# Performance work log

Measured on AMD Instinct MI355X. Metric: run time of the kernel, lower is better.

The kernel has to match this reference:

```python
import jax, jax.numpy as jnp
import numpy as np

IN_DIM, HIDDEN_DIM, LATENT_DIM = 512, 1024, 256
B, N = 64, 1024


def setup_inputs() -> dict:
    key = jax.random.key(0)
    ks = jax.random.split(key, 8)
    x = jax.random.normal(ks[0], (B, N, IN_DIM), dtype=jnp.float32)
    a = jax.random.uniform(ks[1], (B, N, N), dtype=jnp.float32)
    s1 = 1.0 / np.sqrt(IN_DIM)
    s2 = 1.0 / np.sqrt(HIDDEN_DIM)
    W1 = jax.random.uniform(ks[2], (HIDDEN_DIM, IN_DIM), jnp.float32, -s1, s1)
    b1 = jax.random.uniform(ks[3], (HIDDEN_DIM,), jnp.float32, -s1, s1)
    W_mu = jax.random.uniform(ks[4], (LATENT_DIM, HIDDEN_DIM), jnp.float32, -s2, s2)
    b_mu = jax.random.uniform(ks[5], (LATENT_DIM,), jnp.float32, -s2, s2)
    W_lv = jax.random.uniform(ks[6], (LATENT_DIM, HIDDEN_DIM), jnp.float32, -s2, s2)
    b_lv = jax.random.uniform(ks[7], (LATENT_DIM,), jnp.float32, -s2, s2)
    return {"x": x, "a": a, "W1": W1, "b1": b1, "W_mu": W_mu, "b_mu": b_mu,
            "W_lv": W_lv, "b_lv": b_lv}


def normalize_adj(a):
    # A_hat = A + I; D^{-1/2} A_hat D^{-1/2} expressed as row/col scaling
    n = a.shape[-1]
    a_hat = a + jnp.eye(n, dtype=a.dtype)
    deg = a_hat.sum(axis=-1)                      # [B, N]
    d = (deg + 1e-8) ** -0.5                      # [B, N]
    return a_hat * d[..., :, None] * d[..., None, :]


def reference(x, a, W1, b1, W_mu, b_mu, W_lv, b_lv):
    a_norm = normalize_adj(a)                     # [B, N, N]
    h = jnp.einsum('bnm,bmd->bnd', a_norm, x)     # message passing
    h = jax.nn.relu(jnp.einsum('bnd,hd->bnh', h, W1) + b1)
    mu = jnp.einsum('bnh,lh->bnl', h, W_mu) + b_mu
    logvar = jnp.einsum('bnh,lh->bnl', h, W_lv) + b_lv
    return (mu, logvar)
```

## Files before the change

kernel.cpp:

```cpp
#include <hip/hip_runtime.h>
#include <hip/hip_bf16.h>
#include <type_traits>

typedef unsigned short u16;
typedef __attribute__((ext_vector_type(8))) short s16x8;
typedef __attribute__((ext_vector_type(4))) float f32x4;

__device__ __forceinline__ u16 f2bf(float f) {
    union { float f; unsigned u; } c; c.f = f;
    unsigned r = c.u + 0x7fffu + ((c.u >> 16) & 1u);
    return (u16)(r >> 16);
}

__device__ __forceinline__ void gld_lds16(const u16* g, u16* l) {
    __builtin_amdgcn_global_load_lds(
        (const __attribute__((address_space(1))) void*)g,
        (__attribute__((address_space(3))) void*)l, 16, 0, 0);
}

template<bool CVT>
__global__ __launch_bounds__(256) void rowsum_kernel(const float* __restrict__ a,
                                                     float* __restrict__ dsc,
                                                     u16* __restrict__ ab) {
    const int wave = threadIdx.x >> 6, lane = threadIdx.x & 63;
    const long row = (long)blockIdx.x * 4 + wave;
    const int diag = (int)(row & 1023);
    const float4* a4 = (const float4*)(a + row * 1024);
    float s = 0.f;
    #pragma unroll
    for (int i = 0; i < 4; ++i) {
        float4 v = a4[i * 64 + lane];
        s += v.x + v.y + v.z + v.w;
        if (CVT) {
            const int c0 = (i * 64 + lane) * 4;
            float e[4] = {v.x, v.y, v.z, v.w};
            if (diag >= c0 && diag < c0 + 4) e[diag - c0] += 1.0f;
            union { u16 u[4]; uint2 w; } cv;
            cv.u[0] = f2bf(e[0]); cv.u[1] = f2bf(e[1]);
            cv.u[2] = f2bf(e[2]); cv.u[3] = f2bf(e[3]);
            *(uint2*)(ab + row * 1024 + c0) = cv.w;
        }
    }
    #pragma unroll
    for (int off = 32; off > 0; off >>= 1) s += __shfl_down(s, off, 64);
    if (lane == 0) dsc[row] = rsqrtf(s + 1.0f + 1e-8f);
}

__global__ __launch_bounds__(256) void xst_kernel(const float* __restrict__ x,
                                                  const float* __restrict__ dsc,
                                                  u16* __restrict__ xst) {
    __shared__ u16 ls[64][65];
    const int b  = blockIdx.z;
    const int n0 = blockIdx.x * 64;
    const int j0 = blockIdx.y * 64;
    const int t  = threadIdx.x;
    {
        int jj = t >> 4, nn = (t & 15) * 4;
        #pragma unroll
        for (int it = 0; it < 4; ++it, jj += 16) {
            float dj = dsc[b * 1024 + j0 + jj];
            float4 v = *(const float4*)(x + ((long)(b * 1024 + j0 + jj)) * 512 + n0 + nn);
            ls[jj][nn + 0] = f2bf(v.x * dj);
            ls[jj][nn + 1] = f2bf(v.y * dj);
            ls[jj][nn + 2] = f2bf(v.z * dj);
            ls[jj][nn + 3] = f2bf(v.w * dj);
        }
    }
    __syncthreads();
    {
        int nn = t >> 2;
        int jv = (t & 3) * 8;
        #pragma unroll
        for (int it = 0; it < 2; ++it, jv += 32) {
            union { u16 u[8]; uint4 w; } cv;
            #pragma unroll
            for (int u = 0; u < 8; ++u) cv.u[u] = ls[jv + u][nn];
            *(uint4*)(xst + ((long)b * 512 + n0 + nn) * 1024 + j0 + jv) = cv.w;
        }
    }
}

__global__ __launch_bounds__(256) void cvt_weights(const float* __restrict__ W1,
                                                   const float* __restrict__ Wmu,
                                                   const float* __restrict__ Wlv,
                                                   u16* __restrict__ w1b,
                                                   u16* __restrict__ wml) {
    int i = blockIdx.x * 256 + threadIdx.x;
    w1b[i] = f2bf(W1[i]);
    wml[i] = f2bf(i < 262144 ? Wmu[i] : Wlv[i - 262144]);
}

template<int EPI>
__global__ __launch_bounds__(256) void gemm_lds(
    const u16* __restrict__ A, const u16* __restrict__ Bt,
    int K, long aBStride, long bBStride,
    const float* __restrict__ dsc,
    u16* __restrict__ outb,
    const float* __restrict__ bias0, const float* __restrict__ bias1,
    float* __restrict__ outMu, float* __restrict__ outLv)
{
    __shared__ __align__(16) u16 As[128 * 32];
    __shared__ __align__(16) u16 Bs[128 * 32];
    const int bz = blockIdx.z;
    const u16* Ab = A + (long)bz * aBStride;
    const u16* Bb = Bt + (long)bz * bBStride;
    const int n0 = blockIdx.x * 128, m0 = blockIdx.y * 128;
    const int t = threadIdx.x;
    const int wave = t >> 6, lane = t & 63, quad = lane >> 4, tr = lane & 15;
    const int wm = (wave >> 1) * 64, wn = (wave & 1) * 64;

    const int srowA = wave * 32 + (lane >> 2);
    const int scol  = (lane & 3) * 8;
    u16* ldsA0 = As + wave * 1024;
    u16* ldsB0 = Bs + wave * 1024;

    f32x4 acc[4][4];
    #pragma unroll
    for (int i = 0; i < 4; ++i)
        #pragma unroll
        for (int j = 0; j < 4; ++j) acc[i][j] = (f32x4){0.f, 0.f, 0.f, 0.f};

    for (int k0 = 0; k0 < K; k0 += 32) {
        #pragma unroll
        for (int it = 0; it < 2; ++it) {
            gld_lds16(Ab + (long)(m0 + srowA + it * 16) * K + k0 + scol, ldsA0 + it * 512);
            gld_lds16(Bb + (long)(n0 + srowA + it * 16) * K + k0 + scol, ldsB0 + it * 512);
        }
        __syncthreads();
        s16x8 af[4], bfv[4];
        #pragma unroll
        for (int mi = 0; mi < 4; ++mi)
            af[mi] = *(const s16x8*)&As[(wm + mi * 16 + tr) * 32 + quad * 8];
        #pragma unroll
        for (int ni = 0; ni < 4; ++ni)
            bfv[ni] = *(const s16x8*)&Bs[(wn + ni * 16 + tr) * 32 + quad * 8];
        #pragma unroll
        for (int mi = 0; mi < 4; ++mi)
            #pragma unroll
            for (int ni = 0; ni < 4; ++ni)
                acc[mi][ni] = __builtin_amdgcn_mfma_f32_16x16x32_bf16(af[mi], bfv[ni], acc[mi][ni], 0, 0, 0);
        __syncthreads();
    }

    #pragma unroll
    for (int mi = 0; mi < 4; ++mi) {
        #pragma unroll
        for (int ni = 0; ni < 4; ++ni) {
            const int gn = n0 + wn + ni * 16 + tr;
            #pragma unroll
            for (int r = 0; r < 4; ++r) {
                const int gm = m0 + wm + mi * 16 + quad * 4 + r;
                float v = acc[mi][ni][r];
                if constexpr (EPI == 1) {
                    long row = (long)bz * 1024 + gm;
                    outb[row * 512 + gn] = f2bf(dsc[row] * v);
                } else if constexpr (EPI == 2) {
                    float hv = v + bias0[gn];
                    outb[(long)gm * 1024 + gn] = f2bf(hv > 0.f ? hv : 0.f);
                } else {
                    if (gn < 256) outMu[(long)gm * 256 + gn] = v + bias0[gn];
                    else          outLv[(long)gm * 256 + (gn - 256)] = v + bias1[gn - 256];
                }
            }
        }
    }
}

__global__ __launch_bounds__(256) void gemm_f32a(
    const float* __restrict__ A, const u16* __restrict__ Bt,
    const float* __restrict__ dsc, const float* __restrict__ xin,
    u16* __restrict__ outb)
{
    __shared__ __align__(16) u16 As[128 * 40];
    __shared__ __align__(16) u16 Bs[128 * 40];
    const int bz = blockIdx.z;
    const float* Ab = A + (long)bz * 1024 * 1024;
    const u16* Bb = Bt + (long)bz * 512 * 1024;
    const int n0 = blockIdx.x * 128, m0 = blockIdx.y * 128;
    const int t = threadIdx.x;
    const int wave = t >> 6, lane = t & 63, quad = lane >> 4, tr = lane & 15;
    const int wm = (wave >> 1) * 64, wn = (wave & 1) * 64;
    const int K = 1024;

    f32x4 acc[4][4];
    #pragma unroll
    for (int i = 0; i < 4; ++i)
        #pragma unroll
        for (int j = 0; j < 4; ++j) acc[i][j] = (f32x4){0.f, 0.f, 0.f, 0.f};

    const int mm = t >> 2, kk = (t & 3) * 8;
    for (int k0 = 0; k0 < K; k0 += 32) {
        #pragma unroll
        for (int it = 0; it < 2; ++it) {
            const int r = mm + it * 64;
            const float4* p = (const float4*)(Ab + (long)(m0 + r) * K + k0 + kk);
            float4 v0 = p[0], v1 = p[1];
            union { u16 u[8]; uint4 w; } cv;
            cv.u[0]=f2bf(v0.x); cv.u[1]=f2bf(v0.y); cv.u[2]=f2bf(v0.z); cv.u[3]=f2bf(v0.w);
            cv.u[4]=f2bf(v1.x); cv.u[5]=f2bf(v1.y); cv.u[6]=f2bf(v1.z); cv.u[7]=f2bf(v1.w);
            *(uint4*)&As[r * 40 + kk] = cv.w;
            uint4 v = *(const uint4*)(Bb + (long)(n0 + r) * K + k0 + kk);
            *(uint4*)&Bs[r * 40 + kk] = v;
        }
        __syncthreads();
        s16x8 af[4], bfv[4];
        #pragma unroll
        for (int mi = 0; mi < 4; ++mi)
            af[mi] = *(const s16x8*)&As[(wm + mi * 16 + tr) * 40 + quad * 8];
        #pragma unroll
        for (int ni = 0; ni < 4; ++ni)
            bfv[ni] = *(const s16x8*)&Bs[(wn + ni * 16 + tr) * 40 + quad * 8];
        #pragma unroll
        for (int mi = 0; mi < 4; ++mi)
            #pragma unroll
            for (int ni = 0; ni < 4; ++ni)
                acc[mi][ni] = __builtin_amdgcn_mfma_f32_16x16x32_bf16(af[mi], bfv[ni], acc[mi][ni], 0, 0, 0);
        __syncthreads();
    }
    #pragma unroll
    for (int mi = 0; mi < 4; ++mi)
        #pragma unroll
        for (int ni = 0; ni < 4; ++ni) {
            const int gn = n0 + wn + ni * 16 + tr;
            #pragma unroll
            for (int r = 0; r < 4; ++r) {
                const int gm = m0 + wm + mi * 16 + quad * 4 + r;
                long row = (long)bz * 1024 + gm;
                float di = dsc[row];
                outb[row * 512 + gn] = f2bf(di * (acc[mi][ni][r] + di * xin[row * 512 + gn]));
            }
        }
}

extern "C" void kernel_launch(void* const* d_in, const int* in_sizes, int n_in,
                              void* d_out, int out_size, void* d_ws, size_t ws_size,
                              hipStream_t stream) {
    const float* x   = (const float*)d_in[0];
    const float* a   = (const float*)d_in[1];
    const float* W1  = (const float*)d_in[2];
    const float* b1  = (const float*)d_in[3];
    const float* Wmu = (const float*)d_in[4];
    const float* bmu = (const float*)d_in[5];
    const float* Wlv = (const float*)d_in[6];
    const float* blv = (const float*)d_in[7];
    float* out = (float*)d_out;

    char* base = (char*)d_ws;
    size_t off = 0;
    auto take = [&](size_t bytes) { char* p = base + off; off += (bytes + 255) & ~(size_t)255; return p; };
    float* dsc = (float*)take((size_t)65536 * 4);
    u16*  xst  = (u16*)take((size_t)64 * 512 * 1024 * 2);
    u16*  h    = (u16*)take((size_t)65536 * 512 * 2);
    u16*  hid  = (u16*)take((size_t)65536 * 1024 * 2);
    u16*  w1b  = (u16*)take((size_t)1024 * 512 * 2);
    u16*  wml  = (u16*)take((size_t)512 * 1024 * 2);
    u16*  ab   = (u16*)take((size_t)64 * 1024 * 1024 * 2);
    const bool useAb = (off <= ws_size);

    if (useAb) rowsum_kernel<true ><<<16384, 256, 0, stream>>>(a, dsc, ab);
    else       rowsum_kernel<false><<<16384, 256, 0, stream>>>(a, dsc, nullptr);
    xst_kernel<<<dim3(8, 16, 64), 256, 0, stream>>>(x, dsc, xst);
    cvt_weights<<<2048, 256, 0, stream>>>(W1, Wmu, Wlv, w1b, wml);

    if (useAb)
        gemm_lds<1><<<dim3(4, 8, 64), 256, 0, stream>>>(
            ab, xst, 1024, 1024L * 1024, 512L * 1024,
            dsc, h, nullptr, nullptr, nullptr, nullptr);
    else
        gemm_f32a<<<dim3(4, 8, 64), 256, 0, stream>>>(a, xst, dsc, x, h);

    gemm_lds<2><<<dim3(8, 512, 1), 256, 0, stream>>>(
        h, w1b, 512, 0, 0, nullptr, hid, b1, nullptr, nullptr, nullptr);

    gemm_lds<3><<<dim3(4, 512, 1), 256, 0, stream>>>(
        hid, wml, 1024, 0, 0, nullptr, nullptr, bmu, blv,
        out, out + (size_t)65536 * 256);
}
```

Before: 876.7 us.

## Replace 128x128 GEMM with double-buffered 256x256 tile kernel with swizzled LDS

Replaces the single-buffered 128x128 bf16 MFMA GEMM with a 256x256-tile, 512-thread kernel. It double-buffers LDS through direct global-to-LDS loads, so the next K tile is prefetched while MFMAs run, and uses explicit waitcnt, barriers and setprio to order the work. It also XOR-swizzles the LDS columns to avoid bank conflicts and remaps workgroup IDs for cache locality. The epilogues are simplified with hoisted bias and scale loads. Larger tiles raise data reuse but use more registers (128 accumulator floats per lane), add sync points, and launch fewer workgroups.

```diff
diff --git a/kernel.cpp b/kernel.cpp
--- a/kernel.cpp
+++ b/kernel.cpp
@@ -1,6 +1,5 @@
 #include <hip/hip_runtime.h>
 #include <hip/hip_bf16.h>
-#include <type_traits>
 
 typedef unsigned short u16;
 typedef __attribute__((ext_vector_type(8))) short s16x8;
@@ -91,7 +90,7 @@
 }
 
 template<int EPI>
-__global__ __launch_bounds__(256) void gemm_lds(
+__global__ __launch_bounds__(512, 2) void gemm256(
     const u16* __restrict__ A, const u16* __restrict__ Bt,
     int K, long aBStride, long bBStride,
     const float* __restrict__ dsc,
@@ -99,68 +98,155 @@
     const float* __restrict__ bias0, const float* __restrict__ bias1,
     float* __restrict__ outMu, float* __restrict__ outLv)
 {
-    __shared__ __align__(16) u16 As[128 * 32];
-    __shared__ __align__(16) u16 Bs[128 * 32];
-    const int bz = blockIdx.z;
+    __shared__ __align__(16) u16 As[2][256 * 32];
+    __shared__ __align__(16) u16 Bs[2][256 * 32];
+
+    const int gx = gridDim.x, gy = gridDim.y;
+    const int nwg = gx * gy * gridDim.z;
+    const int fid = (blockIdx.z * gy + blockIdx.y) * gx + blockIdx.x;
+    int swz = fid;
+    if (!(nwg & 7)) swz = (fid & 7) * (nwg >> 3) + (fid >> 3);
+    const int bx  = swz % gx;
+    const int tmp = swz / gx;
+    const int by  = tmp % gy;
+    const int bz  = tmp / gy;
+
     const u16* Ab = A + (long)bz * aBStride;
     const u16* Bb = Bt + (long)bz * bBStride;
-    const int n0 = blockIdx.x * 128, m0 = blockIdx.y * 128;
-    const int t = threadIdx.x;
-    const int wave = t >> 6, lane = t & 63, quad = lane >> 4, tr = lane & 15;
-    const int wm = (wave >> 1) * 64, wn = (wave & 1) * 64;
-
-    const int srowA = wave * 32 + (lane >> 2);
-    const int scol  = (lane & 3) * 8;
-    u16* ldsA0 = As + wave * 1024;
-    u16* ldsB0 = Bs + wave * 1024;
-
-    f32x4 acc[4][4];
-    #pragma unroll
-    for (int i = 0; i < 4; ++i)
+    const int n0 = bx * 256, m0 = by * 256;
+    const int T = (int)threadIdx.x;
+    const int wid = T >> 6, lane = T & 63, quad = lane >> 4, tr = lane & 15;
+    const int wm = (wid >> 2) * 128;
+    const int wn = (wid & 3) * 64;
+    const int NT = K >> 5;
+
+    const int sr   = T >> 2;
+    const int scol = ((T & 3) ^ (sr & 3)) << 3;
+    const u16* gA = Ab + (long)(m0 + sr) * K + scol;
+    const u16* gB = Bb + (long)(n0 + sr) * K + scol;
+    const long rowK = (long)128 * K;
+    u16* const wA0 = &As[0][0] + wid * 512;
+    u16* const wB0 = &Bs[0][0] + wid * 512;
+    u16* const wA1 = &As[1][0] + wid * 512;
+    u16* const wB1 = &Bs[1][0] + wid * 512;
+
+    f32x4 acc[8][4];
+    #pragma unroll
+    for (int i = 0; i < 8; ++i)
         #pragma unroll
         for (int j = 0; j < 4; ++j) acc[i][j] = (f32x4){0.f, 0.f, 0.f, 0.f};
 
-    for (int k0 = 0; k0 < K; k0 += 32) {
-        #pragma unroll
-        for (int it = 0; it < 2; ++it) {
-            gld_lds16(Ab + (long)(m0 + srowA + it * 16) * K + k0 + scol, ldsA0 + it * 512);
-            gld_lds16(Bb + (long)(n0 + srowA + it * 16) * K + k0 + scol, ldsB0 + it * 512);
-        }
-        __syncthreads();
+    gld_lds16(gA,           wA0); gld_lds16(gA + rowK,        wA0 + 4096);
+    gld_lds16(gB,           wB0); gld_lds16(gB + rowK,        wB0 + 4096);
+    gld_lds16(gA + 32,      wA1); gld_lds16(gA + 32 + rowK,   wA1 + 4096);
+    gld_lds16(gB + 32,      wB1); gld_lds16(gB + 32 + rowK,   wB1 + 4096);
+    asm volatile("s_waitcnt vmcnt(4)" ::: "memory");
+    __builtin_amdgcn_s_barrier();
+    __builtin_amdgcn_sched_barrier(0);
+
+    const u16* rdA  = &As[0][0]; const u16* rdB  = &Bs[0][0];
+    const u16* rdA2 = &As[1][0]; const u16* rdB2 = &Bs[1][0];
+    u16* stA = wA0; u16* stB = wB0;
+    u16* stA2 = wA1; u16* stB2 = wB1;
+
+    const int rofs = (quad ^ (tr & 3)) << 3;
+    const int rbA  = (wm + tr) * 32 + rofs;
+
+    for (int t = 0; t < NT; ++t) {
         s16x8 af[4], bfv[4];
         #pragma unroll
-        for (int mi = 0; mi < 4; ++mi)
-            af[mi] = *(const s16x8*)&As[(wm + mi * 16 + tr) * 32 + quad * 8];
-        #pragma unroll
-        for (int ni = 0; ni < 4; ++ni)
-            bfv[ni] = *(const s16x8*)&Bs[(wn + ni * 16 + tr) * 32 + quad * 8];
+        for (int i = 0; i < 4; ++i) af[i]  = *(const s16x8*)&rdA[rbA + i * 512];
+        #pragma unroll
+        for (int i = 0; i < 4; ++i) bfv[i] = *(const s16x8*)&rdB[(wn + i * 16 + tr) * 32 + rofs];
+        __builtin_amdgcn_s_barrier();
+        asm volatile("s_waitcnt lgkmcnt(0)" ::: "memory");
+        __builtin_amdgcn_sched_barrier(0);
+        __builtin_amdgcn_s_setprio(1);
         #pragma unroll
         for (int mi = 0; mi < 4; ++mi)
             #pragma unroll
             for (int ni = 0; ni < 4; ++ni)
                 acc[mi][ni] = __builtin_amdgcn_mfma_f32_16x16x32_bf16(af[mi], bfv[ni], acc[mi][ni], 0, 0, 0);
-        __syncthreads();
-    }
-
-    #pragma unroll
-    for (int mi = 0; mi < 4; ++mi) {
-        #pragma unroll
-        for (int ni = 0; ni < 4; ++ni) {
-            const int gn = n0 + wn + ni * 16 + tr;
+        __builtin_amdgcn_s_setprio(0);
+        __builtin_amdgcn_s_barrier();
+        #pragma unroll
+        for (int i = 0; i < 4; ++i) af[i] = *(const s16x8*)&rdA[rbA + 2048 + i * 512];
+        __builtin_amdgcn_s_barrier();
+        asm volatile("s_waitcnt lgkmcnt(0)" ::: "memory");
+        __builtin_amdgcn_sched_barrier(0);
+        __builtin_amdgcn_s_setprio(1);
+        #pragma unroll
+        for (int mi = 0; mi < 4; ++mi)
+            #pragma unroll
+            for (int ni = 0; ni < 4; ++ni)
+                acc[mi + 4][ni] = __builtin_amdgcn_mfma_f32_16x16x32_bf16(af[mi], bfv[ni], acc[mi + 4][ni], 0, 0, 0);
+        __builtin_amdgcn_s_setprio(0);
+        __builtin_amdgcn_s_barrier();
+        __builtin_amdgcn_sched_barrier(0);
+        if (t + 2 < NT) {
+            const u16* a = gA + (long)(t + 2) * 32;
+            const u16* b = gB + (long)(t + 2) * 32;
+            gld_lds16(a, stA); gld_lds16(a + rowK, stA + 4096);
+            gld_lds16(b, stB); gld_lds16(b + rowK, stB + 4096);
+            asm volatile("s_waitcnt vmcnt(4)" ::: "memory");
+        } else if (t + 1 < NT) {
+            asm volatile("s_waitcnt vmcnt(0)" ::: "memory");
+        }
+        __builtin_amdgcn_s_barrier();
+        __builtin_amdgcn_sched_barrier(0);
+        const u16* tA = rdA; rdA = rdA2; rdA2 = tA;
+        const u16* tB = rdB; rdB = rdB2; rdB2 = tB;
+        u16* sA = stA; stA = stA2; stA2 = sA;
+        u16* sB = stB; stB = stB2; stB2 = sB;
+    }
+
+    if constexpr (EPI == 1) {
+        #pragma unroll
+        for (int mi = 0; mi < 8; ++mi) {
+            const int gmB = m0 + wm + mi * 16 + quad * 4;
             #pragma unroll
             for (int r = 0; r < 4; ++r) {
-                const int gm = m0 + wm + mi * 16 + quad * 4 + r;
-                float v = acc[mi][ni][r];
-                if constexpr (EPI == 1) {
-                    long row = (long)bz * 1024 + gm;
-                    outb[row * 512 + gn] = f2bf(dsc[row] * v);
-                } else if constexpr (EPI == 2) {
-                    float hv = v + bias0[gn];
-                    outb[(long)gm * 1024 + gn] = f2bf(hv > 0.f ? hv : 0.f);
-                } else {
-                    if (gn < 256) outMu[(long)gm * 256 + gn] = v + bias0[gn];
-                    else          outLv[(long)gm * 256 + (gn - 256)] = v + bias1[gn - 256];
+                const long row = (long)bz * 1024 + gmB + r;
+                const float d = dsc[row];
+                #pragma unroll
+                for (int ni = 0; ni < 4; ++ni) {
+                    const int gn = n0 + wn + ni * 16 + tr;
+                    outb[row * 512 + gn] = f2bf(d * acc[mi][ni][r]);
                 }
+            }
+        }
+    } else if constexpr (EPI == 2) {
+        float bb[4];
+        #pragma unroll
+        for (int ni = 0; ni < 4; ++ni) bb[ni] = bias0[n0 + wn + ni * 16 + tr];
+        #pragma unroll
+        for (int mi = 0; mi < 8; ++mi) {
+            const long gmB = m0 + wm + mi * 16 + quad * 4;
+            #pragma unroll
+            for (int ni = 0; ni < 4; ++ni) {
+                const int gn = n0 + wn + ni * 16 + tr;
+                #pragma unroll
+                for (int r = 0; r < 4; ++r) {
+                    float hv = acc[mi][ni][r] + bb[ni];
+                    outb[(gmB + r) * 1024 + gn] = f2bf(hv > 0.f ? hv : 0.f);
+                }
+            }
+        }
+    } else {
+        float* op       = (n0 == 0) ? outMu : outLv;
+        const float* bp = (n0 == 0) ? bias0 : bias1;
+        float bb[4];
+        #pragma unroll
+        for (int ni = 0; ni < 4; ++ni) bb[ni] = bp[wn + ni * 16 + tr];
+        #pragma unroll
+        for (int mi = 0; mi < 8; ++mi) {
+            const long gmB = m0 + wm + mi * 16 + quad * 4;
+            #pragma unroll
+            for (int ni = 0; ni < 4; ++ni) {
+                const int cn = wn + ni * 16 + tr;
+                #pragma unroll
+                for (int r = 0; r < 4; ++r)
+                    op[(gmB + r) * 256 + cn] = acc[mi][ni][r] + bb[ni];
             }
         }
     }
@@ -263,16 +349,16 @@
     cvt_weights<<<2048, 256, 0, stream>>>(W1, Wmu, Wlv, w1b, wml);
 
     if (useAb)
-        gemm_lds<1><<<dim3(4, 8, 64), 256, 0, stream>>>(
+        gemm256<1><<<dim3(2, 4, 64), 512, 0, stream>>>(
             ab, xst, 1024, 1024L * 1024, 512L * 1024,
             dsc, h, nullptr, nullptr, nullptr, nullptr);
     else
         gemm_f32a<<<dim3(4, 8, 64), 256, 0, stream>>>(a, xst, dsc, x, h);
 
-    gemm_lds<2><<<dim3(8, 512, 1), 256, 0, stream>>>(
+    gemm256<2><<<dim3(4, 256, 1), 512, 0, stream>>>(
         h, w1b, 512, 0, 0, nullptr, hid, b1, nullptr, nullptr, nullptr);
 
-    gemm_lds<3><<<dim3(4, 512, 1), 256, 0, stream>>>(
+    gemm256<3><<<dim3(2, 256, 1), 512, 0, stream>>>(
         hid, wml, 1024, 0, 0, nullptr, nullptr, bmu, blv,
         out, out + (size_t)65536 * 256);
 }
```

Result: faster. 841.2 us (-4.1%).
